# Kernel optimization log

Measured on AMD Instinct MI355X. Metric: run time of the kernel, lower is better.

## Reference

```python
import math
import jax, jax.numpy as jnp
import numpy as np

H = 16  # num_heads

def get_alibi_slopes(n):
    def pow2_slopes(n):
        start = 2 ** (-2 ** (-(math.log2(n) - 3)))
        return [start * start ** i for i in range(n)]
    if math.log2(n).is_integer():
        return pow2_slopes(n)
    c = 2 ** math.floor(math.log2(n))
    return pow2_slopes(c) + get_alibi_slopes(2 * c)[0::2][: n - c]

def alibi_bias(num_heads, L, dtype=jnp.float32):
    slopes = jnp.asarray(get_alibi_slopes(num_heads), dtype=dtype)  # [H]
    pos = jnp.arange(L)
    rel = (pos[None, :] - pos[:, None]).astype(dtype)               # [L, L] = x - y
    bias = slopes[:, None, None] * rel[None, :, :]                  # [H, L, L]
    causal = pos[None, :] <= pos[:, None]                           # tril mask
    return jnp.where(causal[None, :, :], bias, -jnp.inf)


def setup_inputs() -> dict:
    key = jax.random.key(0)
    ks = jax.random.split(key, 4)
    D = 1024
    B, L = 2, 2048
    s_in = 1.0 / math.sqrt(D)
    return {
        "x": jax.random.normal(ks[0], (B, L, D), dtype=jnp.float32),
        "w_in": jax.random.normal(ks[1], (D, 3 * D), dtype=jnp.float32) * s_in,
        "b_in": jnp.zeros((3 * D,), dtype=jnp.float32),
        "w_out": jax.random.normal(ks[2], (D, D), dtype=jnp.float32) * s_in,
        "b_out": jnp.zeros((D,), dtype=jnp.float32),
    }


def reference(x, w_in, b_in, w_out, b_out):
    B, L, D = x.shape
    dh = D // H
    qkv = x @ w_in + b_in                                   # [B, L, 3D]
    q, k, v = jnp.split(qkv, 3, axis=-1)
    # [B, L, D] -> [B, H, L, dh]
    def heads(t):
        return t.reshape(B, L, H, dh).transpose(0, 2, 1, 3)
    q, k, v = heads(q), heads(k), heads(v)
    scores = jnp.einsum("bhqd,bhkd->bhqk", q, k) / math.sqrt(dh)
    scores = scores + alibi_bias(H, L, scores.dtype)[None]  # [B, H, L, L]
    attn = jax.nn.softmax(scores, axis=-1)
    out = jnp.einsum("bhqk,bhkd->bhqd", attn, v)            # [B, H, L, dh]
    out = out.transpose(0, 2, 1, 3).reshape(B, L, D)
    return out @ w_out + b_out
```

## Files before the change

kernel.cpp:

```cpp
#include <hip/hip_runtime.h>
#include <stdint.h>
#include <math.h>

#define NH 16
#define DH 64
#define SEQ 2048
#define DMODEL 1024

typedef short short8 __attribute__((ext_vector_type(8)));
typedef short short4v __attribute__((ext_vector_type(4)));
typedef float f32x4 __attribute__((ext_vector_type(4)));
typedef __bf16 bf16x4 __attribute__((ext_vector_type(4)));

__device__ __forceinline__ short f2bf(float f) {
  __bf16 h = (__bf16)f;
  return __builtin_bit_cast(short, h);
}
__device__ __forceinline__ short4v cvt4(f32x4 v) {
  bf16x4 b = __builtin_convertvector(v, bf16x4);
  return __builtin_bit_cast(short4v, b);
}
__device__ __forceinline__ float fast_exp2(float x) {
#if __has_builtin(__builtin_amdgcn_exp2f)
  return __builtin_amdgcn_exp2f(x);
#else
  return exp2f(x);
#endif
}

typedef const __attribute__((address_space(1))) uint32_t* gp_t;
typedef __attribute__((address_space(3))) uint32_t* lp_t;
__device__ __forceinline__ void async16(const short* g, short* l) {
  __builtin_amdgcn_global_load_lds((gp_t)g, (lp_t)l, 16, 0, 0);
}

__global__ void k_convert_x(const float* __restrict__ x, short* __restrict__ xb) {
  int i = blockIdx.x * blockDim.x + threadIdx.x;
  f32x4 v = ((const f32x4*)x)[i];
  short4v o;
  o[0] = f2bf(v[0]); o[1] = f2bf(v[1]); o[2] = f2bf(v[2]); o[3] = f2bf(v[3]);
  ((short4v*)xb)[i] = o;
}

__global__ void k_transpose_bf16(const float* __restrict__ in, short* __restrict__ out,
                                 int R, int C) {
  __shared__ float tile[32][33];
  int tx = threadIdx.x, ty = threadIdx.y;
  int c0 = blockIdx.x * 32, r0 = blockIdx.y * 32;
#pragma unroll
  for (int i = 0; i < 4; ++i)
    tile[ty + i * 8][tx] = in[(size_t)(r0 + ty + i * 8) * C + c0 + tx];
  __syncthreads();
#pragma unroll
  for (int i = 0; i < 4; ++i)
    out[(size_t)(c0 + ty + i * 8) * R + r0 + tx] = f2bf(tile[tx][ty + i * 8]);
}

template <int MODE>
__launch_bounds__(256)
__global__ void k_gemm(const short* __restrict__ A, const short* __restrict__ Bt,
                       const float* __restrict__ bias, float* __restrict__ Cf,
                       short* __restrict__ qo, short* __restrict__ ko,
                       short* __restrict__ vo) {
  constexpr int KD = 1024;
  __shared__ __align__(16) short As[128 * 32];
  __shared__ __align__(16) short Bs[128 * 32];
  const int tid = threadIdx.x;
  const int wave = tid >> 6, lane = tid & 63;
  const int quad = lane >> 4, l16 = lane & 15;
  const int wm = wave >> 1, wn = wave & 1;
  const int tM = blockIdx.y * 128, tN = blockIdx.x * 128;

  const int r0 = tid >> 2, cc = (tid & 3) * 8;
  const short* pA0 = A + (size_t)(tM + r0) * KD + cc;
  const short* pA1 = pA0 + (size_t)64 * KD;
  const short* pB0 = Bt + (size_t)(tN + r0) * KD + cc;
  const short* pB1 = pB0 + (size_t)64 * KD;
  short* lA0 = &As[tid * 8];
  short* lA1 = &As[(256 + tid) * 8];
  short* lB0 = &Bs[tid * 8];
  short* lB1 = &Bs[(256 + tid) * 8];

  f32x4 acc[4][4] = {};

  for (int k0 = 0; k0 < KD; k0 += 32) {
    __syncthreads();
    async16(pA0 + k0, lA0);
    async16(pA1 + k0, lA1);
    async16(pB0 + k0, lB0);
    async16(pB1 + k0, lB1);
    __syncthreads();
    short8 af[4], bfr[4];
#pragma unroll
    for (int i = 0; i < 4; ++i)
      af[i] = *(const short8*)&As[(wm * 64 + i * 16 + l16) * 32 + quad * 8];
#pragma unroll
    for (int i = 0; i < 4; ++i)
      bfr[i] = *(const short8*)&Bs[(wn * 64 + i * 16 + l16) * 32 + quad * 8];
#pragma unroll
    for (int i = 0; i < 4; ++i)
#pragma unroll
      for (int j = 0; j < 4; ++j)
        acc[i][j] = __builtin_amdgcn_mfma_f32_16x16x32_bf16(af[i], bfr[j], acc[i][j], 0, 0, 0);
  }

  const int rbase = tM + wm * 64 + quad * 4;
#pragma unroll
  for (int i = 0; i < 4; ++i) {
#pragma unroll
    for (int j = 0; j < 4; ++j) {
      const int col = tN + wn * 64 + j * 16 + l16;
      const float bi = bias[col];
      if (MODE == 0) {
        const int which = col >> 10;
        const int h = (col & 1023) >> 6, d = col & 63;
        if (which == 2) {
          const int row0 = rbase + i * 16;
          const int b = row0 >> 11, li0 = row0 & 2047;
          f32x4 t;
#pragma unroll
          for (int rr = 0; rr < 4; ++rr) t[rr] = acc[i][j][rr] + bi;
          *(short4v*)&vo[(((size_t)(b * NH + h)) * DH + d) * SEQ + li0] = cvt4(t);
        } else {
          short* dst = (which == 0) ? qo : ko;
#pragma unroll
          for (int rr = 0; rr < 4; ++rr) {
            const int row = rbase + i * 16 + rr;
            const int b = row >> 11, li = row & 2047;
            dst[(((size_t)(b * NH + h)) * SEQ + li) * DH + d] = f2bf(acc[i][j][rr] + bi);
          }
        }
      } else {
#pragma unroll
        for (int rr = 0; rr < 4; ++rr) {
          const int row = rbase + i * 16 + rr;
          Cf[(size_t)row * DMODEL + col] = acc[i][j][rr] + bi;
        }
      }
    }
  }
}

__launch_bounds__(256)
__global__ void k_attn(const short* __restrict__ q, const short* __restrict__ k,
                       const short* __restrict__ vt, short* __restrict__ o) {
  __shared__ __align__(16) short Qs[64 * 64];
  __shared__ __align__(16) short Ks[64 * 64];
  __shared__ __align__(16) short Vs[64 * 64];
  __shared__ __align__(16) short Ps[4][16 * 64];
  const int tid = threadIdx.x;
  const int wave = tid >> 6, lane = tid & 63;
  const int quad = lane >> 4, l16 = lane & 15;
  const int sw = l16 & 7;
  const int pairid = blockIdx.x, bh = blockIdx.y;
  const int h = bh & (NH - 1);
  const size_t base = (size_t)bh * SEQ * DH;
  const float LOG2E = 1.44269504088896f;
  const float slope2 = exp2f(-0.5f * (float)(h + 1)) * LOG2E;
  const float scale2 = 0.125f * LOG2E;
  const float FM = 12.0f;

  const int c0i = tid, c1i = 256 + tid;
  const int r0 = c0i >> 3, ch0 = (c0i & 7) ^ (r0 & 7);
  const int r1 = c1i >> 3, ch1 = (c1i & 7) ^ (r1 & 7);
  const int qk_off0 = r0 * DH + ch0 * 8;
  const int qk_off1 = r1 * DH + ch1 * 8;
  const int v_off0 = r0 * SEQ + ch0 * 8;
  const int v_off1 = r1 * SEQ + ch1 * 8;
  short* lQ0 = &Qs[c0i * 8]; short* lQ1 = &Qs[c1i * 8];
  short* lK0 = &Ks[c0i * 8]; short* lK1 = &Ks[c1i * 8];
  short* lV0 = &Vs[c0i * 8]; short* lV1 = &Vs[c1i * 8];

  const int col0 = ((quad ^ sw) << 3);
  const int col1 = col0 ^ 32;
  int psoff[4];
#pragma unroll
  for (int in = 0; in < 4; ++in)
    psoff[in] = l16 * 64 + (((2 * in + (quad >> 1)) ^ sw) << 3) + (quad & 1) * 4;
  const int qlim4 = wave * 16 + l16 - 4 * quad;
  const float s64 = slope2 * 64.0f;
  float rc[4];
#pragma unroll
  for (int r = 0; r < 4; ++r) rc[r] = slope2 * (float)r;

#pragma unroll
  for (int half = 0; half < 2; ++half) {
    const int qt = half ? pairid : (31 - pairid);
    const int q0 = qt * 64;
    __syncthreads();
    {
      const short* qb = q + base + (size_t)q0 * DH;
      async16(qb + qk_off0, lQ0);
      async16(qb + qk_off1, lQ1);
    }
    __syncthreads();
    const short8 qb0 = *(const short8*)&Qs[(wave * 16 + l16) * 64 + col0];
    const short8 qb1 = *(const short8*)&Qs[(wave * 16 + l16) * 64 + col1];

    f32x4 accO[4] = {};
    float lsum = 0.f;
    const int qrow = q0 + wave * 16 + l16;
    const float qoff = -slope2 * (float)qrow - FM + slope2 * (float)(4 * quad);
    float inoff[4];
#pragma unroll
    for (int in = 0; in < 4; ++in)
      inoff[in] = qoff + slope2 * (float)(16 * in);

    const short* kp = k + base;
    const short* vp = vt + base;
    for (int kt = 0; kt <= qt; ++kt) {
      __syncthreads();
      async16(kp + qk_off0, lK0);
      async16(kp + qk_off1, lK1);
      async16(vp + v_off0, lV0);
      async16(vp + v_off1, lV1);
      kp += 64 * DH;
      vp += 64;
      __syncthreads();

      f32x4 s[4];
#pragma unroll
      for (int in = 0; in < 4; ++in) {
        const short8 ka0 = *(const short8*)&Ks[(in * 16 + l16) * 64 + col0];
        const short8 ka1 = *(const short8*)&Ks[(in * 16 + l16) * 64 + col1];
        f32x4 t = {};
        t = __builtin_amdgcn_mfma_f32_16x16x32_bf16(ka0, qb0, t, 0, 0, 0);
        t = __builtin_amdgcn_mfma_f32_16x16x32_bf16(ka1, qb1, t, 0, 0, 0);
        s[in] = t;
      }

      if (kt == qt) {
#pragma unroll
        for (int in = 0; in < 4; ++in) {
          f32x4 p;
#pragma unroll
          for (int r = 0; r < 4; ++r) {
            float val = fast_exp2(fmaf(s[in][r], scale2, inoff[in] + rc[r]));
            val = (16 * in + r <= qlim4) ? val : 0.f;
            p[r] = val;
            lsum += val;
          }
          *(short4v*)&Ps[wave][psoff[in]] = cvt4(p);
        }
      } else {
#pragma unroll
        for (int in = 0; in < 4; ++in) {
          f32x4 p;
#pragma unroll
          for (int r = 0; r < 4; ++r) {
            float val = fast_exp2(fmaf(s[in][r], scale2, inoff[in] + rc[r]));
            p[r] = val;
            lsum += val;
          }
          *(short4v*)&Ps[wave][psoff[in]] = cvt4(p);
        }
      }
#pragma unroll
      for (int in = 0; in < 4; ++in) inoff[in] += s64;

      const short8 pa0 = *(const short8*)&Ps[wave][l16 * 64 + col0];
      const short8 pa1 = *(const short8*)&Ps[wave][l16 * 64 + col1];
#pragma unroll
      for (int i = 0; i < 4; ++i) {
        const short8 va0 = *(const short8*)&Vs[(i * 16 + l16) * 64 + col0];
        const short8 va1 = *(const short8*)&Vs[(i * 16 + l16) * 64 + col1];
        accO[i] = __builtin_amdgcn_mfma_f32_16x16x32_bf16(va0, pa0, accO[i], 0, 0, 0);
        accO[i] = __builtin_amdgcn_mfma_f32_16x16x32_bf16(va1, pa1, accO[i], 0, 0, 0);
      }
    }

    lsum += __shfl_xor(lsum, 16, 64);
    lsum += __shfl_xor(lsum, 32, 64);
    const float inv = 1.0f / lsum;

    const int b = bh >> 4;
    short* ob = o + ((((size_t)b * SEQ + qrow) * NH + h) * DH + 4 * quad);
#pragma unroll
    for (int i = 0; i < 4; ++i) {
      f32x4 t;
#pragma unroll
      for (int r = 0; r < 4; ++r) t[r] = accO[i][r] * inv;
      *(short4v*)&ob[16 * i] = cvt4(t);
    }
  }
}

extern "C" void kernel_launch(void* const* d_in, const int* in_sizes, int n_in,
                              void* d_out, int out_size, void* d_ws, size_t ws_size,
                              hipStream_t stream) {
  const float* x = (const float*)d_in[0];
  const float* w_in = (const float*)d_in[1];
  const float* b_in = (const float*)d_in[2];
  const float* w_out = (const float*)d_in[3];
  const float* b_out = (const float*)d_in[4];
  float* out = (float*)d_out;

  char* ws = (char*)d_ws;
  short* xb = (short*)(ws);
  short* w_in_t = (short*)(ws + (8u << 20));
  short* w_out_t = (short*)(ws + (14u << 20));
  short* qv = (short*)(ws + (16u << 20));
  short* kv = (short*)(ws + (24u << 20));
  short* vv = (short*)(ws + (32u << 20));
  short* ao = (short*)(ws + (40u << 20));

  k_convert_x<<<4096, 256, 0, stream>>>(x, xb);
  k_transpose_bf16<<<dim3(96, 32), dim3(32, 8), 0, stream>>>(w_in, w_in_t, 1024, 3072);
  k_transpose_bf16<<<dim3(32, 32), dim3(32, 8), 0, stream>>>(w_out, w_out_t, 1024, 1024);
  k_gemm<0><<<dim3(24, 32), 256, 0, stream>>>(xb, w_in_t, b_in, nullptr, qv, kv, vv);
  k_attn<<<dim3(16, 32), 256, 0, stream>>>(qv, kv, vv, ao);
  k_gemm<1><<<dim3(8, 32), 256, 0, stream>>>(ao, w_out_t, b_out, out, nullptr, nullptr, nullptr);
}
```

Before: 204.1 us.

## Deepen GEMM K-tile to 64 with swizzled LDS and unpair attention blocks

The GEMM now stages 64-wide K slices into a swizzled LDS layout, which halves the number of barrier pairs per tile and spreads LDS bank accesses. Its launch bounds now request three blocks per CU. The attention kernel drops the paired-tile scheme, where each block handled one long and one short query tile, and launches one block per query tile with the heaviest tiles scheduled first. This doubles the grid for more parallelism and lets the hardware handle load balancing, at the cost of re-staging Q per block and a more uneven per-block workload.

```diff
diff --git a/kernel.cpp b/kernel.cpp
--- a/kernel.cpp
+++ b/kernel.cpp
@@ -57,51 +57,64 @@
 }
 
 template <int MODE>
-__launch_bounds__(256)
+__launch_bounds__(256, 3)
 __global__ void k_gemm(const short* __restrict__ A, const short* __restrict__ Bt,
                        const float* __restrict__ bias, float* __restrict__ Cf,
                        short* __restrict__ qo, short* __restrict__ ko,
                        short* __restrict__ vo) {
   constexpr int KD = 1024;
-  __shared__ __align__(16) short As[128 * 32];
-  __shared__ __align__(16) short Bs[128 * 32];
+  __shared__ __align__(16) short As[128 * 64];
+  __shared__ __align__(16) short Bs[128 * 64];
   const int tid = threadIdx.x;
   const int wave = tid >> 6, lane = tid & 63;
   const int quad = lane >> 4, l16 = lane & 15;
   const int wm = wave >> 1, wn = wave & 1;
   const int tM = blockIdx.y * 128, tN = blockIdx.x * 128;
 
-  const int r0 = tid >> 2, cc = (tid & 3) * 8;
-  const short* pA0 = A + (size_t)(tM + r0) * KD + cc;
-  const short* pA1 = pA0 + (size_t)64 * KD;
-  const short* pB0 = Bt + (size_t)(tN + r0) * KD + cc;
-  const short* pB1 = pB0 + (size_t)64 * KD;
-  short* lA0 = &As[tid * 8];
-  short* lA1 = &As[(256 + tid) * 8];
-  short* lB0 = &Bs[tid * 8];
-  short* lB1 = &Bs[(256 + tid) * 8];
+  const short* pA[4];
+  const short* pB[4];
+  short* lA[4];
+  short* lB[4];
+#pragma unroll
+  for (int t = 0; t < 4; ++t) {
+    const int c = t * 256 + tid;
+    const int row = c >> 3, gch = (c & 7) ^ (row & 7);
+    pA[t] = A + (size_t)(tM + row) * KD + gch * 8;
+    pB[t] = Bt + (size_t)(tN + row) * KD + gch * 8;
+    lA[t] = &As[c * 8];
+    lB[t] = &Bs[c * 8];
+  }
+
+  const int sw = l16 & 7;
+  const int col0 = (quad ^ sw) << 3;
+  const int col1 = col0 ^ 32;
 
   f32x4 acc[4][4] = {};
 
-  for (int k0 = 0; k0 < KD; k0 += 32) {
+  for (int k0 = 0; k0 < KD; k0 += 64) {
     __syncthreads();
-    async16(pA0 + k0, lA0);
-    async16(pA1 + k0, lA1);
-    async16(pB0 + k0, lB0);
-    async16(pB1 + k0, lB1);
+#pragma unroll
+    for (int t = 0; t < 4; ++t) {
+      async16(pA[t] + k0, lA[t]);
+      async16(pB[t] + k0, lB[t]);
+    }
     __syncthreads();
-    short8 af[4], bfr[4];
-#pragma unroll
-    for (int i = 0; i < 4; ++i)
-      af[i] = *(const short8*)&As[(wm * 64 + i * 16 + l16) * 32 + quad * 8];
-#pragma unroll
-    for (int i = 0; i < 4; ++i)
-      bfr[i] = *(const short8*)&Bs[(wn * 64 + i * 16 + l16) * 32 + quad * 8];
-#pragma unroll
-    for (int i = 0; i < 4; ++i)
-#pragma unroll
-      for (int j = 0; j < 4; ++j)
-        acc[i][j] = __builtin_amdgcn_mfma_f32_16x16x32_bf16(af[i], bfr[j], acc[i][j], 0, 0, 0);
+#pragma unroll
+    for (int kh = 0; kh < 2; ++kh) {
+      const int col = kh ? col1 : col0;
+      short8 af[4], bfr[4];
+#pragma unroll
+      for (int i = 0; i < 4; ++i)
+        af[i] = *(const short8*)&As[(wm * 64 + i * 16 + l16) * 64 + col];
+#pragma unroll
+      for (int i = 0; i < 4; ++i)
+        bfr[i] = *(const short8*)&Bs[(wn * 64 + i * 16 + l16) * 64 + col];
+#pragma unroll
+      for (int i = 0; i < 4; ++i)
+#pragma unroll
+        for (int j = 0; j < 4; ++j)
+          acc[i][j] = __builtin_amdgcn_mfma_f32_16x16x32_bf16(af[i], bfr[j], acc[i][j], 0, 0, 0);
+    }
   }
 
   const int rbase = tM + wm * 64 + quad * 4;
@@ -152,7 +165,7 @@
   const int wave = tid >> 6, lane = tid & 63;
   const int quad = lane >> 4, l16 = lane & 15;
   const int sw = l16 & 7;
-  const int pairid = blockIdx.x, bh = blockIdx.y;
+  const int qt = 31 - blockIdx.x, bh = blockIdx.y;
   const int h = bh & (NH - 1);
   const size_t base = (size_t)bh * SEQ * DH;
   const float LOG2E = 1.44269504088896f;
@@ -183,105 +196,100 @@
 #pragma unroll
   for (int r = 0; r < 4; ++r) rc[r] = slope2 * (float)r;
 
-#pragma unroll
-  for (int half = 0; half < 2; ++half) {
-    const int qt = half ? pairid : (31 - pairid);
-    const int q0 = qt * 64;
+  const int q0 = qt * 64;
+  {
+    const short* qb = q + base + (size_t)q0 * DH;
+    async16(qb + qk_off0, lQ0);
+    async16(qb + qk_off1, lQ1);
+  }
+  __syncthreads();
+  const short8 qb0 = *(const short8*)&Qs[(wave * 16 + l16) * 64 + col0];
+  const short8 qb1 = *(const short8*)&Qs[(wave * 16 + l16) * 64 + col1];
+
+  f32x4 accO[4] = {};
+  float lsum = 0.f;
+  const int qrow = q0 + wave * 16 + l16;
+  const float qoff = -slope2 * (float)qrow - FM + slope2 * (float)(4 * quad);
+  float inoff[4];
+#pragma unroll
+  for (int in = 0; in < 4; ++in)
+    inoff[in] = qoff + slope2 * (float)(16 * in);
+
+  const short* kp = k + base;
+  const short* vp = vt + base;
+  for (int kt = 0; kt <= qt; ++kt) {
     __syncthreads();
-    {
-      const short* qb = q + base + (size_t)q0 * DH;
-      async16(qb + qk_off0, lQ0);
-      async16(qb + qk_off1, lQ1);
-    }
+    async16(kp + qk_off0, lK0);
+    async16(kp + qk_off1, lK1);
+    async16(vp + v_off0, lV0);
+    async16(vp + v_off1, lV1);
+    kp += 64 * DH;
+    vp += 64;
     __syncthreads();
-    const short8 qb0 = *(const short8*)&Qs[(wave * 16 + l16) * 64 + col0];
-    const short8 qb1 = *(const short8*)&Qs[(wave * 16 + l16) * 64 + col1];
-
-    f32x4 accO[4] = {};
-    float lsum = 0.f;
-    const int qrow = q0 + wave * 16 + l16;
-    const float qoff = -slope2 * (float)qrow - FM + slope2 * (float)(4 * quad);
-    float inoff[4];
-#pragma unroll
-    for (int in = 0; in < 4; ++in)
-      inoff[in] = qoff + slope2 * (float)(16 * in);
-
-    const short* kp = k + base;
-    const short* vp = vt + base;
-    for (int kt = 0; kt <= qt; ++kt) {
-      __syncthreads();
-      async16(kp + qk_off0, lK0);
-      async16(kp + qk_off1, lK1);
-      async16(vp + v_off0, lV0);
-      async16(vp + v_off1, lV1);
-      kp += 64 * DH;
-      vp += 64;
-      __syncthreads();
-
-      f32x4 s[4];
+
+    f32x4 s[4];
+#pragma unroll
+    for (int in = 0; in < 4; ++in) {
+      const short8 ka0 = *(const short8*)&Ks[(in * 16 + l16) * 64 + col0];
+      const short8 ka1 = *(const short8*)&Ks[(in * 16 + l16) * 64 + col1];
+      f32x4 t = {};
+      t = __builtin_amdgcn_mfma_f32_16x16x32_bf16(ka0, qb0, t, 0, 0, 0);
+      t = __builtin_amdgcn_mfma_f32_16x16x32_bf16(ka1, qb1, t, 0, 0, 0);
+      s[in] = t;
+    }
+
+    if (kt == qt) {
 #pragma unroll
       for (int in = 0; in < 4; ++in) {
-        const short8 ka0 = *(const short8*)&Ks[(in * 16 + l16) * 64 + col0];
-        const short8 ka1 = *(const short8*)&Ks[(in * 16 + l16) * 64 + col1];
-        f32x4 t = {};
-        t = __builtin_amdgcn_mfma_f32_16x16x32_bf16(ka0, qb0, t, 0, 0, 0);
-        t = __builtin_amdgcn_mfma_f32_16x16x32_bf16(ka1, qb1, t, 0, 0, 0);
-        s[in] = t;
+        f32x4 p;
+#pragma unroll
+        for (int r = 0; r < 4; ++r) {
+          float val = fast_exp2(fmaf(s[in][r], scale2, inoff[in] + rc[r]));
+          val = (16 * in + r <= qlim4) ? val : 0.f;
+          p[r] = val;
+          lsum += val;
+        }
+        *(short4v*)&Ps[wave][psoff[in]] = cvt4(p);
       }
-
-      if (kt == qt) {
-#pragma unroll
-        for (int in = 0; in < 4; ++in) {
-          f32x4 p;
-#pragma unroll
-          for (int r = 0; r < 4; ++r) {
-            float val = fast_exp2(fmaf(s[in][r], scale2, inoff[in] + rc[r]));
-            val = (16 * in + r <= qlim4) ? val : 0.f;
-            p[r] = val;
-            lsum += val;
-          }
-          *(short4v*)&Ps[wave][psoff[in]] = cvt4(p);
+    } else {
+#pragma unroll
+      for (int in = 0; in < 4; ++in) {
+        f32x4 p;
+#pragma unroll
+        for (int r = 0; r < 4; ++r) {
+          float val = fast_exp2(fmaf(s[in][r], scale2, inoff[in] + rc[r]));
+          p[r] = val;
+          lsum += val;
         }
-      } else {
-#pragma unroll
-        for (int in = 0; in < 4; ++in) {
-          f32x4 p;
-#pragma unroll
-          for (int r = 0; r < 4; ++r) {
-            float val = fast_exp2(fmaf(s[in][r], scale2, inoff[in] + rc[r]));
-            p[r] = val;
-            lsum += val;
-          }
-          *(short4v*)&Ps[wave][psoff[in]] = cvt4(p);
-        }
+        *(short4v*)&Ps[wave][psoff[in]] = cvt4(p);
       }
-#pragma unroll
-      for (int in = 0; in < 4; ++in) inoff[in] += s64;
-
-      const short8 pa0 = *(const short8*)&Ps[wave][l16 * 64 + col0];
-      const short8 pa1 = *(const short8*)&Ps[wave][l16 * 64 + col1];
-#pragma unroll
-      for (int i = 0; i < 4; ++i) {
-        const short8 va0 = *(const short8*)&Vs[(i * 16 + l16) * 64 + col0];
-        const short8 va1 = *(const short8*)&Vs[(i * 16 + l16) * 64 + col1];
-        accO[i] = __builtin_amdgcn_mfma_f32_16x16x32_bf16(va0, pa0, accO[i], 0, 0, 0);
-        accO[i] = __builtin_amdgcn_mfma_f32_16x16x32_bf16(va1, pa1, accO[i], 0, 0, 0);
-      }
-    }
-
-    lsum += __shfl_xor(lsum, 16, 64);
-    lsum += __shfl_xor(lsum, 32, 64);
-    const float inv = 1.0f / lsum;
-
-    const int b = bh >> 4;
-    short* ob = o + ((((size_t)b * SEQ + qrow) * NH + h) * DH + 4 * quad);
+    }
+#pragma unroll
+    for (int in = 0; in < 4; ++in) inoff[in] += s64;
+
+    const short8 pa0 = *(const short8*)&Ps[wave][l16 * 64 + col0];
+    const short8 pa1 = *(const short8*)&Ps[wave][l16 * 64 + col1];
 #pragma unroll
     for (int i = 0; i < 4; ++i) {
-      f32x4 t;
-#pragma unroll
-      for (int r = 0; r < 4; ++r) t[r] = accO[i][r] * inv;
-      *(short4v*)&ob[16 * i] = cvt4(t);
-    }
+      const short8 va0 = *(const short8*)&Vs[(i * 16 + l16) * 64 + col0];
+      const short8 va1 = *(const short8*)&Vs[(i * 16 + l16) * 64 + col1];
+      accO[i] = __builtin_amdgcn_mfma_f32_16x16x32_bf16(va0, pa0, accO[i], 0, 0, 0);
+      accO[i] = __builtin_amdgcn_mfma_f32_16x16x32_bf16(va1, pa1, accO[i], 0, 0, 0);
+    }
+  }
+
+  lsum += __shfl_xor(lsum, 16, 64);
+  lsum += __shfl_xor(lsum, 32, 64);
+  const float inv = 1.0f / lsum;
+
+  const int b = bh >> 4;
+  short* ob = o + ((((size_t)b * SEQ + qrow) * NH + h) * DH + 4 * quad);
+#pragma unroll
+  for (int i = 0; i < 4; ++i) {
+    f32x4 t;
+#pragma unroll
+    for (int r = 0; r < 4; ++r) t[r] = accO[i][r] * inv;
+    *(short4v*)&ob[16 * i] = cvt4(t);
   }
 }
 
@@ -308,6 +316,6 @@
   k_transpose_bf16<<<dim3(96, 32), dim3(32, 8), 0, stream>>>(w_in, w_in_t, 1024, 3072);
   k_transpose_bf16<<<dim3(32, 32), dim3(32, 8), 0, stream>>>(w_out, w_out_t, 1024, 1024);
   k_gemm<0><<<dim3(24, 32), 256, 0, stream>>>(xb, w_in_t, b_in, nullptr, qv, kv, vv);
-  k_attn<<<dim3(16, 32), 256, 0, stream>>>(qv, kv, vv, ao);
+  k_attn<<<dim3(32, 32), 256, 0, stream>>>(qv, kv, vv, ao);
   k_gemm<1><<<dim3(8, 32), 256, 0, stream>>>(ao, w_out_t, b_out, out, nullptr, nullptr, nullptr);
 }
```

Result: faster. 192.5 us (-5.7%).
